# Kernel optimization log

Measured on AMD Instinct MI355X. Metric: run time of the kernel, lower is better.

## Reference

```python
import jax, jax.numpy as jnp
import numpy as np

N = 100_000      # nodes
E = 1_600_000    # edges
F_IN = 256       # num_node_features
H = 128          # hidden_dim
G = 1_000        # graphs in batch


def setup_inputs() -> dict:
    key = jax.random.key(0)
    ks = jax.random.split(key, 12)
    x = jax.random.normal(ks[0], (N, F_IN), jnp.float32)
    edge_index = jax.random.randint(ks[1], (2, E), 0, N)
    batch = jnp.sort(jax.random.randint(ks[2], (N,), 0, G))
    def w(k, shape):
        fan_in = shape[0]
        return jax.random.normal(k, shape, jnp.float32) / np.sqrt(fan_in)
    return {
        "x": x,
        "edge_index": edge_index,
        "batch": batch,
        "W1": w(ks[3], (F_IN, H)), "b1": jnp.zeros((H,), jnp.float32),
        "W2": w(ks[4], (H, H)),    "b2": jnp.zeros((H,), jnp.float32),
        "W3": w(ks[5], (H, H)),    "b3": jnp.zeros((H,), jnp.float32),
        "fw1": w(ks[6], (H, 32)),  "fb1": jnp.zeros((32,), jnp.float32),
        "fw2": w(ks[7], (32, 2)),  "fb2": jnp.zeros((2,), jnp.float32),
    }


def reference(x, edge_index, batch, W1, b1, W2, b2, W3, b3, fw1, fb1, fw2, fb2):
    # GCN normalization with self-loops (PyG GCNConv defaults)
    loop = jnp.arange(N)
    src = jnp.concatenate([edge_index[0], loop])  # [E+N]
    dst = jnp.concatenate([edge_index[1], loop])
    deg = jax.ops.segment_sum(jnp.ones(E + N, x.dtype), dst, num_segments=N)
    dis = jnp.where(deg > 0, jax.lax.rsqrt(deg), 0.0)
    norm = (dis[src] * dis[dst])[:, None]  # [E+N, 1]

    def gcn(h, W, b):
        h = h @ W                                    # linear transform first (fewer bytes moved)
        msg = h[src] * norm                          # gather + scale
        return jax.ops.segment_sum(msg, dst, num_segments=N) + b  # scatter-add

    h = jax.nn.relu(gcn(x, W1, b1))   # dropout = identity (eval mode)
    h = jax.nn.relu(gcn(h, W2, b2))
    h = jax.nn.relu(gcn(h, W3, b3))

    # global_mean_pool over graph ids
    sums = jax.ops.segment_sum(h, batch, num_segments=G)          # [G, H]
    cnt = jax.ops.segment_sum(jnp.ones(N, h.dtype), batch, num_segments=G)
    g = sums / jnp.maximum(cnt, 1.0)[:, None]

    g = jax.nn.relu(g @ fw1 + fb1)
    logits = g @ fw2 + fb2
    return jax.nn.log_softmax(logits, axis=1)
```

## Files before the change

### kernel.cpp

```cpp
#include <hip/hip_runtime.h>
#include <hip/hip_bf16.h>
#include <math.h>

#define N_NODES 100000
#define N_EDGES 1600000
#define F_IN 256
#define H_DIM 128
#define N_GRAPHS 1000

#define NB_BUCKETS ((N_NODES + 255) >> 8)
#define BSTRIDE 392
#define A_BLOCKS 256
#define EPB (N_EDGES / A_BLOCKS)

typedef unsigned short bfu;
typedef unsigned char u8;
typedef short short8 __attribute__((ext_vector_type(8)));
typedef float f32x4 __attribute__((ext_vector_type(4)));
typedef float f32x2 __attribute__((ext_vector_type(2)));

__device__ __forceinline__ float b2f(unsigned u) {
    union { unsigned int i; float f; } v;
    v.i = u << 16;
    return v.f;
}
__device__ __forceinline__ bfu f2b(float f) {
    __hip_bfloat16 h = __float2bfloat16(f);
    return *reinterpret_cast<bfu*>(&h);
}
__device__ __forceinline__ unsigned pk4_fp8(float v0, float v1, float v2, float v3) {
    int r = __builtin_amdgcn_cvt_pk_fp8_f32(v0, v1, 0, false);
    r = __builtin_amdgcn_cvt_pk_fp8_f32(v2, v3, r, true);
    return (unsigned)r;
}
__device__ __forceinline__ void acc4_fp8(float* a, unsigned v) {
    f32x2 p;
    p = __builtin_amdgcn_cvt_pk_f32_fp8((int)v, false); a[0] += p.x; a[1] += p.y;
    p = __builtin_amdgcn_cvt_pk_f32_fp8((int)v, true);  a[2] += p.x; a[3] += p.y;
}

__global__ __launch_bounds__(256) void k_hist(const int* __restrict__ dst,
                                              int* __restrict__ cnt_bb) {
    __shared__ int h[BSTRIDE];
    const int t = threadIdx.x;
    for (int i = t; i < BSTRIDE; i += 256) h[i] = 0;
    __syncthreads();
    const int base = blockIdx.x * EPB;
    for (int i = t; i < EPB; i += 256) atomicAdd(&h[dst[base + i] >> 8], 1);
    __syncthreads();
    for (int i = t; i < NB_BUCKETS; i += 256) cnt_bb[blockIdx.x * BSTRIDE + i] = h[i];
}

__global__ __launch_bounds__(256) void k_scan_blocks(int* __restrict__ cnt_bb,
                                                     int* __restrict__ btot) {
    __shared__ int s[256];
    const int t = threadIdx.x;
    const int b = blockIdx.x;
    int v = cnt_bb[t * BSTRIDE + b];
    s[t] = v;
    __syncthreads();
    for (int off = 1; off < 256; off <<= 1) {
        int u = (t >= off) ? s[t - off] : 0;
        __syncthreads();
        s[t] += u;
        __syncthreads();
    }
    cnt_bb[t * BSTRIDE + b] = s[t] - v;
    if (t == 255) btot[b] = s[255];
}

__global__ __launch_bounds__(512) void k_scan_buckets(const int* __restrict__ btot,
                                                      int* __restrict__ bucket_base) {
    __shared__ int s[512];
    const int t = threadIdx.x;
    int v = (t < NB_BUCKETS) ? btot[t] : 0;
    s[t] = v;
    __syncthreads();
    for (int off = 1; off < 512; off <<= 1) {
        int u = (t >= off) ? s[t - off] : 0;
        __syncthreads();
        s[t] += u;
        __syncthreads();
    }
    if (t < NB_BUCKETS) bucket_base[t] = s[t] - v;
    if (t == 0) bucket_base[NB_BUCKETS] = N_EDGES;
}

__global__ __launch_bounds__(256) void k_stage(const int* __restrict__ src,
                                               const int* __restrict__ dst,
                                               const int* __restrict__ cnt_bb,
                                               const int* __restrict__ bucket_base,
                                               unsigned* __restrict__ staging) {
    __shared__ int cur[BSTRIDE];
    const int t = threadIdx.x;
    const int blk = blockIdx.x;
    for (int i = t; i < NB_BUCKETS; i += 256)
        cur[i] = bucket_base[i] + cnt_bb[blk * BSTRIDE + i];
    __syncthreads();
    const int base = blk * EPB;
    for (int i = t; i < EPB; i += 256) {
        int d = dst[base + i];
        int s = src[base + i];
        int b = d >> 8;
        int pos = atomicAdd(&cur[b], 1);
        staging[pos] = (unsigned)s | ((unsigned)(d & 255) << 24);
    }
}

__global__ __launch_bounds__(256) void k_bucket(const unsigned* __restrict__ staging,
                                                const int* __restrict__ bucket_base,
                                                int* __restrict__ row_ptr,
                                                float* __restrict__ dis,
                                                int* __restrict__ col) {
    __shared__ int h[256];
    __shared__ int sc[256];
    __shared__ int cur[256];
    const int t = threadIdx.x;
    const int b = blockIdx.x;
    const int s0 = bucket_base[b];
    const int ne = bucket_base[b + 1] - s0;
    h[t] = 0;
    __syncthreads();
    for (int i = t; i < ne; i += 256) atomicAdd(&h[staging[s0 + i] >> 24], 1);
    __syncthreads();
    int myc = h[t];
    sc[t] = myc;
    __syncthreads();
    for (int off = 1; off < 256; off <<= 1) {
        int u = (t >= off) ? sc[t - off] : 0;
        __syncthreads();
        sc[t] += u;
        __syncthreads();
    }
    int excl = sc[t] - myc;
    int node = b * 256 + t;
    if (node <= N_NODES) row_ptr[node] = s0 + excl;
    if (node < N_NODES) dis[node] = rsqrtf((float)(myc + 1));
    cur[t] = s0 + excl;
    __syncthreads();
    for (int i = t; i < ne; i += 256) {
        unsigned u = staging[s0 + i];
        int pos = atomicAdd(&cur[u >> 24], 1);
        col[pos] = (int)(u & 0xFFFFFFu);
    }
}

__device__ __forceinline__ void wpack_one(const float* __restrict__ W,
                                          bfu* __restrict__ Wp, int u) {
    int lane = u & 63;
    int nf = (u >> 6) & 7;
    int ks = u >> 9;
    int k = ks * 32 + (lane >> 4) * 8;
    int n = nf * 16 + (lane & 15);
    bfu o[8];
#pragma unroll
    for (int j = 0; j < 8; ++j) o[j] = f2b(W[(k + j) * 128 + n]);
    uint4 pk;
    pk.x = (unsigned)o[0] | ((unsigned)o[1] << 16);
    pk.y = (unsigned)o[2] | ((unsigned)o[3] << 16);
    pk.z = (unsigned)o[4] | ((unsigned)o[5] << 16);
    pk.w = (unsigned)o[6] | ((unsigned)o[7] << 16);
    *(uint4*)&Wp[u * 8] = pk;
}

__global__ __launch_bounds__(256) void k_misc(const float* __restrict__ W1,
                                              const float* __restrict__ W2,
                                              const float* __restrict__ W3,
                                              bfu* __restrict__ wp1, bfu* __restrict__ wp2,
                                              bfu* __restrict__ wp3,
                                              const int* __restrict__ batch,
                                              int* __restrict__ bounds) {
    const int b = blockIdx.x, t = threadIdx.x;
    if (b < 16) {
        wpack_one(W1, wp1, b * 256 + t);
    } else if (b < 24) {
        wpack_one(W2, wp2, (b - 16) * 256 + t);
    } else if (b < 32) {
        wpack_one(W3, wp3, (b - 24) * 256 + t);
    } else {
        int g = (b - 32) * 256 + t;
        if (g <= N_GRAPHS) {
            int lo = 0, hi = N_NODES;
            while (lo < hi) {
                int mid = (lo + hi) >> 1;
                if (batch[mid] < g) lo = mid + 1; else hi = mid;
            }
            bounds[g] = lo;
        }
    }
}

__global__ __launch_bounds__(256, 2) void k_mm1(const float* __restrict__ A,
                                                const bfu* __restrict__ Wp,
                                                const float* __restrict__ dis,
                                                u8* __restrict__ C8, int M) {
    const int t = threadIdx.x;
    const int w = t >> 6, l = t & 63, l15 = l & 15, lhi = l >> 4;
    const int row = blockIdx.x * 64 + w * 16 + l15;
    const int rowc = row < M ? row : M - 1;
    const float* ap = A + (long)rowc * 256 + lhi * 8;

    float4 va[8][2];
#pragma unroll
    for (int ks = 0; ks < 8; ++ks) {
        va[ks][0] = *(const float4*)(ap + ks * 32);
        va[ks][1] = *(const float4*)(ap + ks * 32 + 4);
    }
    __builtin_amdgcn_sched_barrier(0);

    f32x4 acc[8];
#pragma unroll
    for (int nf = 0; nf < 8; ++nf) acc[nf] = (f32x4)0.0f;

#pragma unroll
    for (int ks = 0; ks < 8; ++ks) {
        unsigned p0 = (unsigned)f2b(va[ks][0].x) | ((unsigned)f2b(va[ks][0].y) << 16);
        unsigned p1 = (unsigned)f2b(va[ks][0].z) | ((unsigned)f2b(va[ks][0].w) << 16);
        unsigned p2 = (unsigned)f2b(va[ks][1].x) | ((unsigned)f2b(va[ks][1].y) << 16);
        unsigned p3 = (unsigned)f2b(va[ks][1].z) | ((unsigned)f2b(va[ks][1].w) << 16);
        uint4 afu = make_uint4(p0, p1, p2, p3);
        short8 af = *(short8*)&afu;
        const bfu* wp = Wp + ((long)(ks * 8) * 64 + l) * 8;
#pragma unroll
        for (int nf = 0; nf < 8; ++nf) {
            short8 wf = *(const short8*)(wp + (long)nf * 64 * 8);
            acc[nf] = __builtin_amdgcn_mfma_f32_16x16x32_bf16(wf, af, acc[nf], 0, 0, 0);
        }
    }
    if (row < M) {
        float sc = dis[row];
        int nb0 = lhi * 4;
#pragma unroll
        for (int nf = 0; nf < 8; ++nf) {
            unsigned pk = pk4_fp8(acc[nf][0] * sc, acc[nf][1] * sc,
                                  acc[nf][2] * sc, acc[nf][3] * sc);
            *(unsigned*)&C8[(long)row * 128 + nf * 16 + nb0] = pk;
        }
    }
}

__global__ __launch_bounds__(256) void k_agg8(const int* __restrict__ row_ptr,
                                              const int* __restrict__ col,
                                              const float* __restrict__ dis,
                                              const u8* __restrict__ t8,
                                              const float* __restrict__ b,
                                              bfu* __restrict__ h) {
    const int t = threadIdx.x;
    const int node = blockIdx.x * 8 + (t >> 5);
    const int lane = t & 31;
    if (node >= N_NODES) return;
    const int q = lane << 2;

    const u8* tp = t8 + q;
    float a[4] = {0.f, 0.f, 0.f, 0.f};
    acc4_fp8(a, *(const unsigned*)&tp[(long)node * 128]);

    int e = row_ptr[node];
    const int end = row_ptr[node + 1];
    for (; e + 7 < end; e += 8) {
        unsigned v[8];
#pragma unroll
        for (int j = 0; j < 8; ++j) v[j] = *(const unsigned*)&tp[(long)col[e + j] * 128];
#pragma unroll
        for (int j = 0; j < 8; ++j) acc4_fp8(a, v[j]);
    }
    for (; e + 3 < end; e += 4) {
        unsigned v0 = *(const unsigned*)&tp[(long)col[e] * 128];
        unsigned v1 = *(const unsigned*)&tp[(long)col[e + 1] * 128];
        unsigned v2 = *(const unsigned*)&tp[(long)col[e + 2] * 128];
        unsigned v3 = *(const unsigned*)&tp[(long)col[e + 3] * 128];
        acc4_fp8(a, v0); acc4_fp8(a, v1); acc4_fp8(a, v2); acc4_fp8(a, v3);
    }
    for (; e < end; ++e)
        acc4_fp8(a, *(const unsigned*)&tp[(long)col[e] * 128]);

    const float dn = dis[node];
    float4 bb = *(const float4*)&b[q];
    float o0 = fmaxf(a[0] * dn + bb.x, 0.0f);
    float o1 = fmaxf(a[1] * dn + bb.y, 0.0f);
    float o2 = fmaxf(a[2] * dn + bb.z, 0.0f);
    float o3 = fmaxf(a[3] * dn + bb.w, 0.0f);
    uint2 pk;
    pk.x = (unsigned)f2b(o0) | ((unsigned)f2b(o1) << 16);
    pk.y = (unsigned)f2b(o2) | ((unsigned)f2b(o3) << 16);
    *(uint2*)&h[(long)node * 128 + q] = pk;
}

__global__ __launch_bounds__(256) void k_mm2(const bfu* __restrict__ A,
                                             const bfu* __restrict__ Wp,
                                             const float* __restrict__ dis,
                                             u8* __restrict__ C8, int M) {
    __shared__ bfu As[2][64 * 40];
    const int t = threadIdx.x;
    const int w = t >> 6;
    const int l = t & 63;
    const int l15 = l & 15;
    const int lhi = l >> 4;
    const int row0 = blockIdx.x * 64;

    f32x4 acc[8];
#pragma unroll
    for (int nf = 0; nf < 8; ++nf) acc[nf] = (f32x4)0.0f;

    uint4 pb = make_uint4(0u, 0u, 0u, 0u);
    {
        int r = t >> 2, s = t & 3;
        if (row0 + r < M) pb = *(const uint4*)&A[(long)(row0 + r) * 128 + s * 8];
    }

    int buf = 0;
#pragma unroll
    for (int ks = 0; ks < 4; ++ks) {
        *(uint4*)&As[buf][(t >> 2) * 40 + (t & 3) * 8] = pb;
        if (ks + 1 < 4) {
            const int k0n = (ks + 1) * 32;
            int r = t >> 2, s = t & 3;
            pb = make_uint4(0u, 0u, 0u, 0u);
            if (row0 + r < M) pb = *(const uint4*)&A[(long)(row0 + r) * 128 + k0n + s * 8];
        }
        __syncthreads();
        short8 af = *(const short8*)&As[buf][(w * 16 + l15) * 40 + lhi * 8];
        const bfu* wp = Wp + ((long)(ks * 8) * 64 + l) * 8;
#pragma unroll
        for (int nf = 0; nf < 8; ++nf) {
            short8 wf = *(const short8*)(wp + (long)nf * 64 * 8);
            acc[nf] = __builtin_amdgcn_mfma_f32_16x16x32_bf16(wf, af, acc[nf], 0, 0, 0);
        }
        if (ks + 1 < 4) __syncthreads();
        buf ^= 1;
    }
    int row = row0 + w * 16 + l15;
    if (row < M) {
        float sc = dis[row];
        int nb0 = lhi * 4;
#pragma unroll
        for (int nf = 0; nf < 8; ++nf) {
            unsigned pko = pk4_fp8(acc[nf][0] * sc, acc[nf][1] * sc,
                                   acc[nf][2] * sc, acc[nf][3] * sc);
            *(unsigned*)&C8[(long)row * 128 + nf * 16 + nb0] = pko;
        }
    }
}

__global__ __launch_bounds__(128) void k_pool_head(const int* __restrict__ bounds,
                                                   const bfu* __restrict__ h,
                                                   const float* __restrict__ fw1, const float* __restrict__ fb1,
                                                   const float* __restrict__ fw2, const float* __restrict__ fb2,
                                                   float* __restrict__ out) {
    const int g = blockIdx.x;
    const int t = threadIdx.x;
    const int s = bounds[g], e = bounds[g + 1];
    float sum = 0.0f;
    int n = s;
    for (; n + 1 < e; n += 2) {
        sum += b2f(h[(long)n * 128 + t]);
        sum += b2f(h[(long)(n + 1) * 128 + t]);
    }
    if (n < e) sum += b2f(h[(long)n * 128 + t]);

    __shared__ float sg[128];
    __shared__ float sh[32];
    float inv = 1.0f / fmaxf((float)(e - s), 1.0f);
    sg[t] = sum * inv;
    __syncthreads();
    if (t < 32) {
        float a = fb1[t];
#pragma unroll 8
        for (int k = 0; k < 128; ++k) a += sg[k] * fw1[k * 32 + t];
        sh[t] = fmaxf(a, 0.0f);
    }
    __syncthreads();
    if (t == 0) {
        float l0 = fb2[0], l1 = fb2[1];
        for (int k = 0; k < 32; ++k) {
            l0 += sh[k] * fw2[k * 2];
            l1 += sh[k] * fw2[k * 2 + 1];
        }
        float m = fmaxf(l0, l1);
        float lse = m + logf(expf(l0 - m) + expf(l1 - m));
        out[g * 2 + 0] = l0 - lse;
        out[g * 2 + 1] = l1 - lse;
    }
}

extern "C" void kernel_launch(void* const* d_in, const int* in_sizes, int n_in,
                              void* d_out, int out_size, void* d_ws, size_t ws_size,
                              hipStream_t stream) {
    const float* x  = (const float*)d_in[0];
    const int* ei   = (const int*)d_in[1];
    const int* batch = (const int*)d_in[2];
    const float* W1 = (const float*)d_in[3];
    const float* b1 = (const float*)d_in[4];
    const float* W2 = (const float*)d_in[5];
    const float* b2 = (const float*)d_in[6];
    const float* W3 = (const float*)d_in[7];
    const float* b3 = (const float*)d_in[8];
    const float* fw1 = (const float*)d_in[9];
    const float* fb1 = (const float*)d_in[10];
    const float* fw2 = (const float*)d_in[11];
    const float* fb2 = (const float*)d_in[12];
    float* out = (float*)d_out;

    const int* src = ei;
    const int* dst = ei + N_EDGES;

    char* ws = (char*)d_ws;
    int*      cnt_bb      = (int*)ws;
    int*      btot        = cnt_bb + A_BLOCKS * BSTRIDE;
    int*      bucket_base = btot + BSTRIDE;
    unsigned* staging     = (unsigned*)(bucket_base + BSTRIDE + 8);
    int*      row_ptr     = (int*)(staging + N_EDGES);
    float*    dis         = (float*)(row_ptr + N_NODES + 4);
    int*      col         = (int*)(dis + N_NODES);
    int*      bounds      = col + N_EDGES;
    bfu*      wpack1      = (bfu*)(bounds + N_GRAPHS + 8);
    bfu*      wpack2      = wpack1 + 32768;
    bfu*      wpack3      = wpack2 + 16384;
    u8*       bufT8       = (u8*)(wpack3 + 16384);
    bfu*      bufH        = (bfu*)(bufT8 + (long)N_NODES * 128);

    k_hist<<<A_BLOCKS, 256, 0, stream>>>(dst, cnt_bb);
    k_scan_blocks<<<NB_BUCKETS, 256, 0, stream>>>(cnt_bb, btot);
    k_scan_buckets<<<1, 512, 0, stream>>>(btot, bucket_base);
    k_stage<<<A_BLOCKS, 256, 0, stream>>>(src, dst, cnt_bb, bucket_base, staging);
    k_bucket<<<NB_BUCKETS, 256, 0, stream>>>(staging, bucket_base, row_ptr, dis, col);
    k_misc<<<36, 256, 0, stream>>>(W1, W2, W3, wpack1, wpack2, wpack3, batch, bounds);

    const int mm1Grid = (N_NODES + 63) / 64;
    const int mm2Grid = (N_NODES + 63) / 64;
    const int aggGrid = (N_NODES + 7) / 8;

    k_mm1<<<mm1Grid, 256, 0, stream>>>(x, wpack1, dis, bufT8, N_NODES);
    k_agg8<<<aggGrid, 256, 0, stream>>>(row_ptr, col, dis, bufT8, b1, bufH);
    k_mm2<<<mm2Grid, 256, 0, stream>>>(bufH, wpack2, dis, bufT8, N_NODES);
    k_agg8<<<aggGrid, 256, 0, stream>>>(row_ptr, col, dis, bufT8, b2, bufH);
    k_mm2<<<mm2Grid, 256, 0, stream>>>(bufH, wpack3, dis, bufT8, N_NODES);
    k_agg8<<<aggGrid, 256, 0, stream>>>(row_ptr, col, dis, bufT8, b3, bufH);

    k_pool_head<<<N_GRAPHS, 128, 0, stream>>>(bounds, bufH, fw1, fb1, fw2, fb2, out);
}
```

Baseline: 305.1 us.

## Store intermediate hidden activations in fp8, merge bucket scan into misc kernel

```diff
diff --git a/kernel.cpp b/kernel.cpp
--- a/kernel.cpp
+++ b/kernel.cpp
@@ -38,6 +38,18 @@
     p = __builtin_amdgcn_cvt_pk_f32_fp8((int)v, false); a[0] += p.x; a[1] += p.y;
     p = __builtin_amdgcn_cvt_pk_f32_fp8((int)v, true);  a[2] += p.x; a[3] += p.y;
 }
+__device__ __forceinline__ uint4 fp8x8_to_bf16x8(uint2 v) {
+    f32x2 p0 = __builtin_amdgcn_cvt_pk_f32_fp8((int)v.x, false);
+    f32x2 p1 = __builtin_amdgcn_cvt_pk_f32_fp8((int)v.x, true);
+    f32x2 p2 = __builtin_amdgcn_cvt_pk_f32_fp8((int)v.y, false);
+    f32x2 p3 = __builtin_amdgcn_cvt_pk_f32_fp8((int)v.y, true);
+    uint4 o;
+    o.x = (unsigned)f2b(p0.x) | ((unsigned)f2b(p0.y) << 16);
+    o.y = (unsigned)f2b(p1.x) | ((unsigned)f2b(p1.y) << 16);
+    o.z = (unsigned)f2b(p2.x) | ((unsigned)f2b(p2.y) << 16);
+    o.w = (unsigned)f2b(p3.x) | ((unsigned)f2b(p3.y) << 16);
+    return o;
+}
 
 __global__ __launch_bounds__(256) void k_hist(const int* __restrict__ dst,
                                               int* __restrict__ cnt_bb) {
@@ -67,23 +79,6 @@
     }
     cnt_bb[t * BSTRIDE + b] = s[t] - v;
     if (t == 255) btot[b] = s[255];
-}
-
-__global__ __launch_bounds__(512) void k_scan_buckets(const int* __restrict__ btot,
-                                                      int* __restrict__ bucket_base) {
-    __shared__ int s[512];
-    const int t = threadIdx.x;
-    int v = (t < NB_BUCKETS) ? btot[t] : 0;
-    s[t] = v;
-    __syncthreads();
-    for (int off = 1; off < 512; off <<= 1) {
-        int u = (t >= off) ? s[t - off] : 0;
-        __syncthreads();
-        s[t] += u;
-        __syncthreads();
-    }
-    if (t < NB_BUCKETS) bucket_base[t] = s[t] - v;
-    if (t == 0) bucket_base[NB_BUCKETS] = N_EDGES;
 }
 
 __global__ __launch_bounds__(256) void k_stage(const int* __restrict__ src,
@@ -169,7 +164,9 @@
                                               bfu* __restrict__ wp1, bfu* __restrict__ wp2,
                                               bfu* __restrict__ wp3,
                                               const int* __restrict__ batch,
-                                              int* __restrict__ bounds) {
+                                              int* __restrict__ bounds,
+                                              const int* __restrict__ btot,
+                                              int* __restrict__ bucket_base) {
     const int b = blockIdx.x, t = threadIdx.x;
     if (b < 16) {
         wpack_one(W1, wp1, b * 256 + t);
@@ -177,7 +174,7 @@
         wpack_one(W2, wp2, (b - 16) * 256 + t);
     } else if (b < 32) {
         wpack_one(W3, wp3, (b - 24) * 256 + t);
-    } else {
+    } else if (b < 36) {
         int g = (b - 32) * 256 + t;
         if (g <= N_GRAPHS) {
             int lo = 0, hi = N_NODES;
@@ -187,6 +184,24 @@
             }
             bounds[g] = lo;
         }
+    } else {
+        __shared__ int s[256];
+        int g0 = 2 * t, g1 = 2 * t + 1;
+        int v0 = (g0 < NB_BUCKETS) ? btot[g0] : 0;
+        int v1 = (g1 < NB_BUCKETS) ? btot[g1] : 0;
+        int pair = v0 + v1;
+        s[t] = pair;
+        __syncthreads();
+        for (int off = 1; off < 256; off <<= 1) {
+            int u = (t >= off) ? s[t - off] : 0;
+            __syncthreads();
+            s[t] += u;
+            __syncthreads();
+        }
+        int excl = s[t] - pair;
+        if (g0 < NB_BUCKETS) bucket_base[g0] = excl;
+        if (g1 < NB_BUCKETS) bucket_base[g1] = excl + v0;
+        if (t == 0) bucket_base[NB_BUCKETS] = N_EDGES;
     }
 }
 
@@ -200,24 +215,29 @@
     const int rowc = row < M ? row : M - 1;
     const float* ap = A + (long)rowc * 256 + lhi * 8;
 
-    float4 va[8][2];
+    float4 buf[4][2];
+#pragma unroll
+    for (int i = 0; i < 4; ++i) {
+        buf[i][0] = *(const float4*)(ap + i * 32);
+        buf[i][1] = *(const float4*)(ap + i * 32 + 4);
+    }
+
+    f32x4 acc[8];
+#pragma unroll
+    for (int nf = 0; nf < 8; ++nf) acc[nf] = (f32x4)0.0f;
+
 #pragma unroll
     for (int ks = 0; ks < 8; ++ks) {
-        va[ks][0] = *(const float4*)(ap + ks * 32);
-        va[ks][1] = *(const float4*)(ap + ks * 32 + 4);
-    }
-    __builtin_amdgcn_sched_barrier(0);
-
-    f32x4 acc[8];
-#pragma unroll
-    for (int nf = 0; nf < 8; ++nf) acc[nf] = (f32x4)0.0f;
-
-#pragma unroll
-    for (int ks = 0; ks < 8; ++ks) {
-        unsigned p0 = (unsigned)f2b(va[ks][0].x) | ((unsigned)f2b(va[ks][0].y) << 16);
-        unsigned p1 = (unsigned)f2b(va[ks][0].z) | ((unsigned)f2b(va[ks][0].w) << 16);
-        unsigned p2 = (unsigned)f2b(va[ks][1].x) | ((unsigned)f2b(va[ks][1].y) << 16);
-        unsigned p3 = (unsigned)f2b(va[ks][1].z) | ((unsigned)f2b(va[ks][1].w) << 16);
+        float4 c0 = buf[ks & 3][0];
+        float4 c1 = buf[ks & 3][1];
+        if (ks + 4 < 8) {
+            buf[ks & 3][0] = *(const float4*)(ap + (ks + 4) * 32);
+            buf[ks & 3][1] = *(const float4*)(ap + (ks + 4) * 32 + 4);
+        }
+        unsigned p0 = (unsigned)f2b(c0.x) | ((unsigned)f2b(c0.y) << 16);
+        unsigned p1 = (unsigned)f2b(c0.z) | ((unsigned)f2b(c0.w) << 16);
+        unsigned p2 = (unsigned)f2b(c1.x) | ((unsigned)f2b(c1.y) << 16);
+        unsigned p3 = (unsigned)f2b(c1.z) | ((unsigned)f2b(c1.w) << 16);
         uint4 afu = make_uint4(p0, p1, p2, p3);
         short8 af = *(short8*)&afu;
         const bfu* wp = Wp + ((long)(ks * 8) * 64 + l) * 8;
@@ -239,12 +259,14 @@
     }
 }
 
+template <bool OUT_BF16>
 __global__ __launch_bounds__(256) void k_agg8(const int* __restrict__ row_ptr,
                                               const int* __restrict__ col,
                                               const float* __restrict__ dis,
                                               const u8* __restrict__ t8,
                                               const float* __restrict__ b,
-                                              bfu* __restrict__ h) {
+                                              bfu* __restrict__ h16,
+                                              u8* __restrict__ h8) {
     const int t = threadIdx.x;
     const int node = blockIdx.x * 8 + (t >> 5);
     const int lane = t & 31;
@@ -280,13 +302,17 @@
     float o1 = fmaxf(a[1] * dn + bb.y, 0.0f);
     float o2 = fmaxf(a[2] * dn + bb.z, 0.0f);
     float o3 = fmaxf(a[3] * dn + bb.w, 0.0f);
-    uint2 pk;
-    pk.x = (unsigned)f2b(o0) | ((unsigned)f2b(o1) << 16);
-    pk.y = (unsigned)f2b(o2) | ((unsigned)f2b(o3) << 16);
-    *(uint2*)&h[(long)node * 128 + q] = pk;
-}
-
-__global__ __launch_bounds__(256) void k_mm2(const bfu* __restrict__ A,
+    if (OUT_BF16) {
+        uint2 pk;
+        pk.x = (unsigned)f2b(o0) | ((unsigned)f2b(o1) << 16);
+        pk.y = (unsigned)f2b(o2) | ((unsigned)f2b(o3) << 16);
+        *(uint2*)&h16[(long)node * 128 + q] = pk;
+    } else {
+        *(unsigned*)&h8[(long)node * 128 + q] = pk4_fp8(o0, o1, o2, o3);
+    }
+}
+
+__global__ __launch_bounds__(256) void k_mm2(const u8* __restrict__ A8,
                                              const bfu* __restrict__ Wp,
                                              const float* __restrict__ dis,
                                              u8* __restrict__ C8, int M) {
@@ -302,21 +328,21 @@
 #pragma unroll
     for (int nf = 0; nf < 8; ++nf) acc[nf] = (f32x4)0.0f;
 
-    uint4 pb = make_uint4(0u, 0u, 0u, 0u);
+    uint2 pb = make_uint2(0u, 0u);
     {
         int r = t >> 2, s = t & 3;
-        if (row0 + r < M) pb = *(const uint4*)&A[(long)(row0 + r) * 128 + s * 8];
+        if (row0 + r < M) pb = *(const uint2*)&A8[(long)(row0 + r) * 128 + s * 8];
     }
 
     int buf = 0;
 #pragma unroll
     for (int ks = 0; ks < 4; ++ks) {
-        *(uint4*)&As[buf][(t >> 2) * 40 + (t & 3) * 8] = pb;
+        *(uint4*)&As[buf][(t >> 2) * 40 + (t & 3) * 8] = fp8x8_to_bf16x8(pb);
         if (ks + 1 < 4) {
             const int k0n = (ks + 1) * 32;
             int r = t >> 2, s = t & 3;
-            pb = make_uint4(0u, 0u, 0u, 0u);
-            if (row0 + r < M) pb = *(const uint4*)&A[(long)(row0 + r) * 128 + k0n + s * 8];
+            pb = make_uint2(0u, 0u);
+            if (row0 + r < M) pb = *(const uint2*)&A8[(long)(row0 + r) * 128 + k0n + s * 8];
         }
         __syncthreads();
         short8 af = *(const short8*)&As[buf][(w * 16 + l15) * 40 + lhi * 8];
@@ -417,25 +443,26 @@
     bfu*      wpack2      = wpack1 + 32768;
     bfu*      wpack3      = wpack2 + 16384;
     u8*       bufT8       = (u8*)(wpack3 + 16384);
-    bfu*      bufH        = (bfu*)(bufT8 + (long)N_NODES * 128);
+    u8*       bufH8       = bufT8 + (long)N_NODES * 128;
+    bfu*      bufH        = (bfu*)(bufH8 + (long)N_NODES * 128);
 
     k_hist<<<A_BLOCKS, 256, 0, stream>>>(dst, cnt_bb);
     k_scan_blocks<<<NB_BUCKETS, 256, 0, stream>>>(cnt_bb, btot);
-    k_scan_buckets<<<1, 512, 0, stream>>>(btot, bucket_base);
+    k_misc<<<37, 256, 0, stream>>>(W1, W2, W3, wpack1, wpack2, wpack3, batch, bounds,
+                                   btot, bucket_base);
     k_stage<<<A_BLOCKS, 256, 0, stream>>>(src, dst, cnt_bb, bucket_base, staging);
     k_bucket<<<NB_BUCKETS, 256, 0, stream>>>(staging, bucket_base, row_ptr, dis, col);
-    k_misc<<<36, 256, 0, stream>>>(W1, W2, W3, wpack1, wpack2, wpack3, batch, bounds);
 
     const int mm1Grid = (N_NODES + 63) / 64;
     const int mm2Grid = (N_NODES + 63) / 64;
     const int aggGrid = (N_NODES + 7) / 8;
 
     k_mm1<<<mm1Grid, 256, 0, stream>>>(x, wpack1, dis, bufT8, N_NODES);
-    k_agg8<<<aggGrid, 256, 0, stream>>>(row_ptr, col, dis, bufT8, b1, bufH);
-    k_mm2<<<mm2Grid, 256, 0, stream>>>(bufH, wpack2, dis, bufT8, N_NODES);
-    k_agg8<<<aggGrid, 256, 0, stream>>>(row_ptr, col, dis, bufT8, b2, bufH);
-    k_mm2<<<mm2Grid, 256, 0, stream>>>(bufH, wpack3, dis, bufT8, N_NODES);
-    k_agg8<<<aggGrid, 256, 0, stream>>>(row_ptr, col, dis, bufT8, b3, bufH);
+    k_agg8<false><<<aggGrid, 256, 0, stream>>>(row_ptr, col, dis, bufT8, b1, nullptr, bufH8);
+    k_mm2<<<mm2Grid, 256, 0, stream>>>(bufH8, wpack2, dis, bufT8, N_NODES);
+    k_agg8<false><<<aggGrid, 256, 0, stream>>>(row_ptr, col, dis, bufT8, b2, nullptr, bufH8);
+    k_mm2<<<mm2Grid, 256, 0, stream>>>(bufH8, wpack3, dis, bufT8, N_NODES);
+    k_agg8<true><<<aggGrid, 256, 0, stream>>>(row_ptr, col, dis, bufT8, b3, bufH, nullptr);
 
     k_pool_head<<<N_GRAPHS, 128, 0, stream>>>(bounds, bufH, fw1, fb1, fw2, fb2, out);
 }
```

Measured after the change: 302.2 us. No clear change (-1.0%).
